# Optimization experiments

Measured on AMD Instinct MI355X. Metric: run time of the kernel, lower is better.

The kernel has to match this reference:

```python
import jax, jax.numpy as jnp
import numpy as np

NUM_HEADS = 32
NUM_KV_HEADS = 8
HEAD_DIM = 128
ROPE_THETA = 10000.0
HIDDEN = NUM_HEADS * HEAD_DIM


def setup_inputs() -> dict:
    key = jax.random.key(0)
    ks = jax.random.split(key, 5)
    B, S = 2, 2048
    hidden_states = jax.random.normal(ks[0], (B, S, HIDDEN), dtype=jnp.float32)
    wq = jax.random.normal(ks[1], (HIDDEN, HIDDEN), dtype=jnp.float32) * 0.02
    wk = jax.random.normal(ks[2], (NUM_KV_HEADS * HEAD_DIM, HIDDEN), dtype=jnp.float32) * 0.02
    wv = jax.random.normal(ks[3], (NUM_KV_HEADS * HEAD_DIM, HIDDEN), dtype=jnp.float32) * 0.02
    wo = jax.random.normal(ks[4], (HIDDEN, HIDDEN), dtype=jnp.float32) * 0.02
    position_ids = jnp.broadcast_to(jnp.arange(S, dtype=jnp.int64 if jax.config.read('jax_enable_x64') else jnp.int32)[None, :], (B, S))
    return {"hidden_states": hidden_states, "position_ids": position_ids,
            "wq": wq, "wk": wk, "wv": wv, "wo": wo}


def _rotate_half(x):
    x1, x2 = jnp.split(x, 2, axis=-1)
    return jnp.concatenate((-x2, x1), axis=-1)


def _rope_tables(position_ids, dtype):
    # inv_freq: [head_dim/2]
    inv_freq = 1.0 / (ROPE_THETA ** (jnp.arange(0, HEAD_DIM, 2, dtype=jnp.float32) / HEAD_DIM))
    # freqs per position: [B, S, head_dim/2] -> emb [B, S, head_dim]
    freqs = position_ids.astype(jnp.float32)[..., None] * inv_freq  # bsd2
    emb = jnp.concatenate((freqs, freqs), axis=-1)
    # unsqueeze head dim -> [B, 1, S, head_dim]
    return jnp.cos(emb).astype(dtype)[:, None], jnp.sin(emb).astype(dtype)[:, None]


def reference(hidden_states, position_ids, wq, wk, wv, wo):
    B, S, H = hidden_states.shape
    n_rep = NUM_HEADS // NUM_KV_HEADS
    # projections (torch Linear: x @ W^T)
    q = (hidden_states @ wq.T).reshape(B, S, NUM_HEADS, HEAD_DIM).transpose(0, 2, 1, 3)
    k = (hidden_states @ wk.T).reshape(B, S, NUM_KV_HEADS, HEAD_DIM).transpose(0, 2, 1, 3)
    v = (hidden_states @ wv.T).reshape(B, S, NUM_KV_HEADS, HEAD_DIM).transpose(0, 2, 1, 3)
    cos, sin = _rope_tables(position_ids, hidden_states.dtype)
    q = q * cos + _rotate_half(q) * sin
    k = k * cos + _rotate_half(k) * sin
    # repeat_kv: [B, kvH, S, D] -> [B, H, S, D]
    k = jnp.repeat(k, n_rep, axis=1)
    v = jnp.repeat(v, n_rep, axis=1)
    scale = 1.0 / jnp.sqrt(jnp.asarray(HEAD_DIM, dtype=hidden_states.dtype))
    scores = jnp.einsum('bhqd,bhkd->bhqk', q, k) * scale
    causal = jnp.tril(jnp.ones((S, S), dtype=bool))
    scores = jnp.where(causal[None, None], scores, jnp.finfo(scores.dtype).min)
    # softmax in fp32 then cast back (matches HF upcast)
    attn = jax.nn.softmax(scores.astype(jnp.float32), axis=-1).astype(q.dtype)
    out = jnp.einsum('bhqk,bhkd->bhqd', attn, v)
    out = out.transpose(0, 2, 1, 3).reshape(B, S, H)
    return out @ wo.T
```

## Files before the change

kernel.cpp:

```cpp
#include <hip/hip_runtime.h>
#include <stdint.h>

#define NH      32
#define NKVH    8
#define HD      128
#define BATCH   2
#define SEQ     2048
#define HIDDEN  4096
#define KVDIM   1024
#define TOKENS  (BATCH*SEQ)

typedef __bf16 bf16x8 __attribute__((ext_vector_type(8)));
typedef float  f32x4  __attribute__((ext_vector_type(4)));

__device__ __forceinline__ uint16_t f32_to_bf16(float f) {
  union { float f; uint32_t u; } v; v.f = f;
  uint32_t r = v.u + 0x7FFFu + ((v.u >> 16) & 1u);
  return (uint16_t)(r >> 16);
}
__device__ __forceinline__ float bf16_to_f32(uint16_t h) {
  union { uint32_t u; float f; } v; v.u = ((uint32_t)h) << 16;
  return v.f;
}
__device__ __forceinline__ bf16x8 ld_frag(const uint16_t* p) {
  return *(const bf16x8*)p;
}
#define MFMA_BF16(a,b,c) __builtin_amdgcn_mfma_f32_16x16x32_bf16((a),(b),(c),0,0,0)
#define NEG_BIG (-1.0e30f)

typedef __attribute__((address_space(1))) void as1_void;
typedef __attribute__((address_space(3))) void as3_void;
__device__ __forceinline__ void gload_lds16(const void* g, void* l) {
  __builtin_amdgcn_global_load_lds((as1_void*)g, (as3_void*)l, 16, 0, 0);
}

__device__ __forceinline__ void cvt8(const float* __restrict__ s,
                                     uint16_t* __restrict__ d, size_t i) {
  const float4* sp = (const float4*)s + 2*i;
  float4 a = sp[0], b = sp[1];
  union { uint16_t u[8]; uint4 v; } o;
  o.u[0]=f32_to_bf16(a.x); o.u[1]=f32_to_bf16(a.y);
  o.u[2]=f32_to_bf16(a.z); o.u[3]=f32_to_bf16(a.w);
  o.u[4]=f32_to_bf16(b.x); o.u[5]=f32_to_bf16(b.y);
  o.u[6]=f32_to_bf16(b.z); o.u[7]=f32_to_bf16(b.w);
  ((uint4*)d)[i] = o.v;
}

__global__ __launch_bounds__(256) void cvt_all(
    const float* __restrict__ X,  const float* __restrict__ Wq,
    const float* __restrict__ Wk, const float* __restrict__ Wv,
    uint16_t* __restrict__ R0, uint16_t* __restrict__ R1,
    uint16_t* __restrict__ R2, uint16_t* __restrict__ R3)
{
  int blk = blockIdx.x;
  const float* s; uint16_t* d; int b0;
  if (blk < 8192)       { s = X;  d = R0; b0 = 0; }
  else if (blk < 16384) { s = Wq; d = R1; b0 = 8192; }
  else if (blk < 18432) { s = Wk; d = R2; b0 = 16384; }
  else                  { s = Wv; d = R3; b0 = 18432; }
  cvt8(s, d, (size_t)(blk - b0)*256 + threadIdx.x);
}

__global__ __launch_bounds__(256) void cvt_one(
    const float* __restrict__ s, uint16_t* __restrict__ d)
{
  cvt8(s, d, (size_t)blockIdx.x*256 + threadIdx.x);
}

__device__ __forceinline__ void store_c(uint16_t* p, float v) { *p = f32_to_bf16(v); }
__device__ __forceinline__ void store_c(float*    p, float v) { *p = v; }

template <typename TC>
__device__ __forceinline__ void gemm_body(
    const uint16_t* __restrict__ A, const uint16_t* __restrict__ B,
    TC* __restrict__ C, int m0, int n0, int N, int K)
{
  __shared__ __align__(16) uint16_t As[3][128*32];
  __shared__ __align__(16) uint16_t Bs[3][128*32];
  const int tid  = threadIdx.x;
  const int wave = tid >> 6;
  const int lane = tid & 63;
  const int wm = (wave >> 1) * 64;
  const int wn = (wave & 1) * 64;
  const int srow = lane >> 2;
  const int scol = (((lane & 3) ^ ((lane >> 3) & 3)) * 8);
  const uint16_t* Ap = A + (size_t)(m0 + wave*16 + srow) * K + scol;
  const uint16_t* Bp = B + (size_t)(n0 + wave*16 + srow) * K + scol;
  const int wuo = wave*16*32;
  const int fr = lane & 15;
  const int fo = (((lane >> 4) ^ ((fr >> 1) & 3)) * 8);
  const int NT = K / 32;

  #pragma unroll
  for (int t = 0; t < 2; ++t) {
    gload_lds16(Ap + (size_t)t*32,                &As[t][wuo]);
    gload_lds16(Ap + (size_t)64*K + (size_t)t*32, &As[t][64*32 + wuo]);
    gload_lds16(Bp + (size_t)t*32,                &Bs[t][wuo]);
    gload_lds16(Bp + (size_t)64*K + (size_t)t*32, &Bs[t][64*32 + wuo]);
  }

  f32x4 acc[4][4] = {};
  int s_cur = 0, s_stage = 2;
  for (int t = 0; t < NT; ++t) {
    if (t < NT - 1) asm volatile("s_waitcnt vmcnt(4)" ::: "memory");
    else            asm volatile("s_waitcnt vmcnt(0)" ::: "memory");
    __builtin_amdgcn_s_barrier();
    asm volatile("" ::: "memory");

    if (t + 2 < NT) {
      const size_t k2 = (size_t)(t + 2) * 32;
      gload_lds16(Ap + k2,                &As[s_stage][wuo]);
      gload_lds16(Ap + (size_t)64*K + k2, &As[s_stage][64*32 + wuo]);
      gload_lds16(Bp + k2,                &Bs[s_stage][wuo]);
      gload_lds16(Bp + (size_t)64*K + k2, &Bs[s_stage][64*32 + wuo]);
    }

    const uint16_t* Asb = As[s_cur];
    const uint16_t* Bsb = Bs[s_cur];
    bf16x8 af[4], bfr[4];
    #pragma unroll
    for (int i = 0; i < 4; ++i) af[i]  = ld_frag(&Asb[(wm + i*16 + fr)*32 + fo]);
    #pragma unroll
    for (int j = 0; j < 4; ++j) bfr[j] = ld_frag(&Bsb[(wn + j*16 + fr)*32 + fo]);
    __builtin_amdgcn_s_setprio(1);
    #pragma unroll
    for (int i = 0; i < 4; ++i)
      #pragma unroll
      for (int j = 0; j < 4; ++j)
        acc[i][j] = MFMA_BF16(af[i], bfr[j], acc[i][j]);
    __builtin_amdgcn_s_setprio(0);

    s_cur   = (s_cur   == 2) ? 0 : s_cur + 1;
    s_stage = (s_stage == 2) ? 0 : s_stage + 1;
  }

  const int cr = (lane >> 4) * 4;
  const int cfr = lane & 15;
  #pragma unroll
  for (int i = 0; i < 4; ++i)
    #pragma unroll
    for (int j = 0; j < 4; ++j)
      #pragma unroll
      for (int r = 0; r < 4; ++r)
        store_c(&C[(size_t)(m0 + wm + i*16 + cr + r) * N + (n0 + wn + j*16 + cfr)],
                acc[i][j][r]);
}

__global__ __launch_bounds__(256, 3) void qkv_gemm(
    const uint16_t* __restrict__ X,
    const uint16_t* __restrict__ Wq, const uint16_t* __restrict__ Wk,
    const uint16_t* __restrict__ Wv,
    uint16_t* __restrict__ Qo, uint16_t* __restrict__ Ko, uint16_t* __restrict__ Vo)
{
  int bx = blockIdx.x;
  const uint16_t* B; uint16_t* C; int n0, N;
  if (bx < 32)      { B = Wq; C = Qo; n0 = bx*128;      N = HIDDEN; }
  else if (bx < 40) { B = Wk; C = Ko; n0 = (bx-32)*128; N = KVDIM;  }
  else              { B = Wv; C = Vo; n0 = (bx-40)*128; N = KVDIM;  }
  gemm_body<uint16_t>(X, B, C, blockIdx.y*128, n0, N, HIDDEN);
}

__global__ __launch_bounds__(256, 3) void out_gemm(
    const uint16_t* __restrict__ A, const uint16_t* __restrict__ B,
    float* __restrict__ C, int N, int K)
{
  gemm_body<float>(A, B, C, blockIdx.y*128, blockIdx.x*128, N, K);
}

__global__ __launch_bounds__(256) void rope_kernel(
    uint16_t* __restrict__ Q, uint16_t* __restrict__ K)
{
  int idx = blockIdx.x * 256 + threadIdx.x;
  int j = idx & 63;
  int rest = idx >> 6;
  int h = rest % (NH + NKVH);
  int t = rest / (NH + NKVH);
  float pos = (float)(t % SEQ);
  float inv_freq = __exp10f(-0.0625f * (float)j);
  float ang = pos * inv_freq;
  float s, c;
  __sincosf(ang, &s, &c);
  uint16_t* base = (h < NH) ? (Q + (size_t)t*HIDDEN + h*HD)
                            : (K + (size_t)t*KVDIM + (h-NH)*HD);
  float x1 = bf16_to_f32(base[j]);
  float x2 = bf16_to_f32(base[j+64]);
  base[j]    = f32_to_bf16(x1*c - x2*s);
  base[j+64] = f32_to_bf16(x2*c + x1*s);
}

__global__ __launch_bounds__(256) void transpose_v(
    const uint16_t* __restrict__ V, uint16_t* __restrict__ Vt)
{
  __shared__ uint16_t tile[64][66];
  int bh = blockIdx.z;  int b = bh >> 3, h = bh & 7;
  int s0 = blockIdx.x * 64;
  int d0 = blockIdx.y * 64;
  int tx = threadIdx.x & 63;
  int ty = threadIdx.x >> 6;
  const uint16_t* Vp = V + (size_t)b*SEQ*KVDIM + (size_t)h*HD;
  for (int r = ty; r < 64; r += 4)
    tile[r][tx] = Vp[(size_t)(s0 + r)*KVDIM + d0 + tx];
  __syncthreads();
  uint16_t* Vtp = Vt + ((size_t)b*NKVH + h)*HD*SEQ;
  for (int r = ty; r < 64; r += 4)
    Vtp[(size_t)(d0 + r)*SEQ + s0 + tx] = tile[tx][r];
}

#define KSTR 136
#define VSTR 72

__global__ __launch_bounds__(256, 4) void flash_attn(
    uint16_t* __restrict__ Q, const uint16_t* __restrict__ K,
    const uint16_t* __restrict__ Vt)
{
  __shared__ __align__(16) uint16_t Ks[64*KSTR];
  __shared__ __align__(16) uint16_t Vs[128*VSTR];
  uint16_t* Ps = Ks;

  const int tid  = threadIdx.x;
  const int wave = tid >> 6;
  const int lane = tid & 63;
  const int fr = lane & 15;
  const int g  = lane >> 4;
  const int fo = g * 8;
  const int bh = blockIdx.y;
  const int b = bh >> 5, h = bh & 31;
  const int kvh = h >> 2;

  uint16_t*       Qh = Q  + (size_t)b*SEQ*HIDDEN + (size_t)h*HD;
  const uint16_t* Kp = K  + (size_t)b*SEQ*KVDIM  + (size_t)kvh*HD;
  const uint16_t* Vp = Vt + ((size_t)b*NKVH + kvh)*HD*SEQ;

  #pragma unroll
  for (int pass = 0; pass < 2; ++pass) {
    const int qt = pass ? (31 - (int)blockIdx.x) : (int)blockIdx.x;
    const int q0 = qt * 64;
    const int qrow = q0 + wave*16 + fr;
    const int orow_base = q0 + wave*16 + g*4;

    bf16x8 qf[4];
    #pragma unroll
    for (int ks = 0; ks < 4; ++ks)
      qf[ks] = ld_frag(Qh + (size_t)(q0 + wave*16 + fr)*HIDDEN + ks*32 + fo);

    float m_i = NEG_BIG, l_i = 0.f;
    f32x4 oacc[8] = {};

    const int nkt = qt + 1;
    for (int kt = 0; kt < nkt; ++kt) {
      const int k0 = kt * 64;
      __syncthreads();
      #pragma unroll
      for (int i = 0; i < 4; ++i) {
        int gi = tid + i*256;
        int kr = gi >> 4, kc = (gi & 15) * 8;
        *(bf16x8*)&Ks[kr*KSTR + kc] = *(const bf16x8*)(Kp + (size_t)(k0 + kr)*KVDIM + kc);
        int vr = gi >> 3, vc = (gi & 7) * 8;
        *(bf16x8*)&Vs[vr*VSTR + vc] = *(const bf16x8*)(Vp + (size_t)vr*SEQ + k0 + vc);
      }
      __syncthreads();

      f32x4 sacc[4] = {};
      #pragma unroll
      for (int ks = 0; ks < 4; ++ks) {
        bf16x8 bk[4];
        #pragma unroll
        for (int j = 0; j < 4; ++j) bk[j] = ld_frag(&Ks[(j*16 + fr)*KSTR + ks*32 + fo]);
        __builtin_amdgcn_s_setprio(1);
        #pragma unroll
        for (int j = 0; j < 4; ++j) sacc[j] = MFMA_BF16(bk[j], qf[ks], sacc[j]);
        __builtin_amdgcn_s_setprio(0);
      }

      const bool diag = (kt == qt);
      #pragma unroll
      for (int j = 0; j < 4; ++j)
        #pragma unroll
        for (int r = 0; r < 4; ++r) {
          float v = sacc[j][r] * 0.08838834764831845f;
          if (diag && (k0 + j*16 + g*4 + r > qrow)) v = NEG_BIG;
          sacc[j][r] = v;
        }

      float mt = sacc[0][0];
      #pragma unroll
      for (int j = 0; j < 4; ++j)
        #pragma unroll
        for (int r = 0; r < 4; ++r)
          if (j | r) mt = fmaxf(mt, sacc[j][r]);
      mt = fmaxf(mt, __shfl_xor(mt, 16, 64));
      mt = fmaxf(mt, __shfl_xor(mt, 32, 64));

      float alpha = 1.0f;
      if (!__all(mt <= m_i + 8.0f)) {
        float mn = fmaxf(m_i, mt);
        alpha = __expf(m_i - mn);
        m_i = mn;
        #pragma unroll
        for (int r = 0; r < 4; ++r) {
          float ar = __shfl(alpha, g*4 + r, 64);
          #pragma unroll
          for (int n = 0; n < 8; ++n) oacc[n][r] *= ar;
        }
      }

      float lt = 0.f;
      uint2 pw[4];
      #pragma unroll
      for (int j = 0; j < 4; ++j) {
        float p0 = __expf(sacc[j][0] - m_i);
        float p1 = __expf(sacc[j][1] - m_i);
        float p2 = __expf(sacc[j][2] - m_i);
        float p3 = __expf(sacc[j][3] - m_i);
        lt += (p0 + p1) + (p2 + p3);
        union { uint16_t u[4]; uint2 v; } pk;
        pk.u[0] = f32_to_bf16(p0); pk.u[1] = f32_to_bf16(p1);
        pk.u[2] = f32_to_bf16(p2); pk.u[3] = f32_to_bf16(p3);
        pw[j] = pk.v;
      }
      lt += __shfl_xor(lt, 16, 64);
      lt += __shfl_xor(lt, 32, 64);
      l_i = l_i * alpha + lt;

      __syncthreads();

      #pragma unroll
      for (int j = 0; j < 4; ++j)
        *(uint2*)&Ps[(wave*16 + fr)*VSTR + j*16 + g*4] = pw[j];

      #pragma unroll
      for (int ks = 0; ks < 2; ++ks) {
        bf16x8 ap = ld_frag(&Ps[(wave*16 + fr)*VSTR + ks*32 + fo]);
        #pragma unroll
        for (int half = 0; half < 2; ++half) {
          bf16x8 bv[4];
          #pragma unroll
          for (int n = 0; n < 4; ++n)
            bv[n] = ld_frag(&Vs[((half*4 + n)*16 + fr)*VSTR + ks*32 + fo]);
          __builtin_amdgcn_s_setprio(1);
          #pragma unroll
          for (int n = 0; n < 4; ++n)
            oacc[half*4 + n] = MFMA_BF16(ap, bv[n], oacc[half*4 + n]);
          __builtin_amdgcn_s_setprio(0);
        }
      }
    }

    #pragma unroll
    for (int r = 0; r < 4; ++r) {
      float lr = __shfl(l_i, g*4 + r, 64);
      float inv_l = 1.0f / lr;
      #pragma unroll
      for (int n = 0; n < 8; ++n)
        Qh[(size_t)(orow_base + r)*HIDDEN + n*16 + fr] = f32_to_bf16(oacc[n][r] * inv_l);
    }
    __syncthreads();
  }
}

extern "C" void kernel_launch(void* const* d_in, const int* in_sizes, int n_in,
                              void* d_out, int out_size, void* d_ws, size_t ws_size,
                              hipStream_t stream)
{
  (void)in_sizes; (void)n_in; (void)out_size; (void)ws_size;
  const float* hidden = (const float*)d_in[0];
  const float* wq = (const float*)d_in[2];
  const float* wk = (const float*)d_in[3];
  const float* wv = (const float*)d_in[4];
  const float* wo = (const float*)d_in[5];
  float* out = (float*)d_out;

  uint16_t* R0 = (uint16_t*)d_ws;
  uint16_t* R1 = R0 + (size_t)HIDDEN*HIDDEN;
  uint16_t* R2 = R1 + (size_t)HIDDEN*HIDDEN;
  uint16_t* R3 = R2 + (size_t)KVDIM*HIDDEN;
  uint16_t* Qb = R3 + (size_t)KVDIM*HIDDEN;
  uint16_t* Kb = Qb + (size_t)TOKENS*HIDDEN;
  uint16_t* Vb = Kb + (size_t)TOKENS*KVDIM;

  dim3 blk(256);
  cvt_all<<<dim3(20480), blk, 0, stream>>>(hidden, wq, wk, wv, R0, R1, R2, R3);
  qkv_gemm<<<dim3(48, TOKENS/128), blk, 0, stream>>>(R0, R1, R2, R3, Qb, Kb, Vb);
  rope_kernel<<<dim3(TOKENS*(NH+NKVH)*64/256), blk, 0, stream>>>(Qb, Kb);
  cvt_one<<<dim3(HIDDEN*HIDDEN/8/256), blk, 0, stream>>>(wo, R0);
  transpose_v<<<dim3(SEQ/64, HD/64, BATCH*NKVH), blk, 0, stream>>>(Vb, R1);
  flash_attn<<<dim3(16, BATCH*NH), blk, 0, stream>>>(Qb, Kb, R1);
  out_gemm<<<dim3(HIDDEN/128, TOKENS/128), blk, 0, stream>>>(Qb, R0, out, HIDDEN, HIDDEN);
}
```

Measured before the change: 802.0 us.

## Use double-buffered GEMM body with higher occupancy for output projection

```diff
diff --git a/kernel.cpp b/kernel.cpp
--- a/kernel.cpp
+++ b/kernel.cpp
@@ -146,6 +146,75 @@
                 acc[i][j][r]);
 }
 
+template <typename TC>
+__device__ __forceinline__ void gemm_body2(
+    const uint16_t* __restrict__ A, const uint16_t* __restrict__ B,
+    TC* __restrict__ C, int m0, int n0, int N, int K)
+{
+  __shared__ __align__(16) uint16_t As[2][128*32];
+  __shared__ __align__(16) uint16_t Bs[2][128*32];
+  const int tid  = threadIdx.x;
+  const int wave = tid >> 6;
+  const int lane = tid & 63;
+  const int wm = (wave >> 1) * 64;
+  const int wn = (wave & 1) * 64;
+  const int srow = lane >> 2;
+  const int scol = (((lane & 3) ^ ((lane >> 3) & 3)) * 8);
+  const uint16_t* Ap = A + (size_t)(m0 + wave*16 + srow) * K + scol;
+  const uint16_t* Bp = B + (size_t)(n0 + wave*16 + srow) * K + scol;
+  const int wuo = wave*16*32;
+  const int fr = lane & 15;
+  const int fo = (((lane >> 4) ^ ((fr >> 1) & 3)) * 8);
+  const int NT = K / 32;
+
+  gload_lds16(Ap,                &As[0][wuo]);
+  gload_lds16(Ap + (size_t)64*K, &As[0][64*32 + wuo]);
+  gload_lds16(Bp,                &Bs[0][wuo]);
+  gload_lds16(Bp + (size_t)64*K, &Bs[0][64*32 + wuo]);
+
+  f32x4 acc[4][4] = {};
+  for (int t = 0; t < NT; ++t) {
+    asm volatile("s_waitcnt vmcnt(0)" ::: "memory");
+    __builtin_amdgcn_s_barrier();
+    asm volatile("" ::: "memory");
+
+    if (t + 1 < NT) {
+      const int s = (t + 1) & 1;
+      const size_t k1 = (size_t)(t + 1) * 32;
+      gload_lds16(Ap + k1,                &As[s][wuo]);
+      gload_lds16(Ap + (size_t)64*K + k1, &As[s][64*32 + wuo]);
+      gload_lds16(Bp + k1,                &Bs[s][wuo]);
+      gload_lds16(Bp + (size_t)64*K + k1, &Bs[s][64*32 + wuo]);
+    }
+
+    const uint16_t* Asb = As[t & 1];
+    const uint16_t* Bsb = Bs[t & 1];
+    bf16x8 af[4], bfr[4];
+    #pragma unroll
+    for (int i = 0; i < 4; ++i) af[i]  = ld_frag(&Asb[(wm + i*16 + fr)*32 + fo]);
+    #pragma unroll
+    for (int j = 0; j < 4; ++j) bfr[j] = ld_frag(&Bsb[(wn + j*16 + fr)*32 + fo]);
+    __builtin_amdgcn_s_setprio(1);
+    #pragma unroll
+    for (int i = 0; i < 4; ++i)
+      #pragma unroll
+      for (int j = 0; j < 4; ++j)
+        acc[i][j] = MFMA_BF16(af[i], bfr[j], acc[i][j]);
+    __builtin_amdgcn_s_setprio(0);
+  }
+
+  const int cr = (lane >> 4) * 4;
+  const int cfr = lane & 15;
+  #pragma unroll
+  for (int i = 0; i < 4; ++i)
+    #pragma unroll
+    for (int j = 0; j < 4; ++j)
+      #pragma unroll
+      for (int r = 0; r < 4; ++r)
+        store_c(&C[(size_t)(m0 + wm + i*16 + cr + r) * N + (n0 + wn + j*16 + cfr)],
+                acc[i][j][r]);
+}
+
 __global__ __launch_bounds__(256, 3) void qkv_gemm(
     const uint16_t* __restrict__ X,
     const uint16_t* __restrict__ Wq, const uint16_t* __restrict__ Wk,
@@ -160,11 +229,11 @@
   gemm_body<uint16_t>(X, B, C, blockIdx.y*128, n0, N, HIDDEN);
 }
 
-__global__ __launch_bounds__(256, 3) void out_gemm(
+__global__ __launch_bounds__(256, 4) void out_gemm(
     const uint16_t* __restrict__ A, const uint16_t* __restrict__ B,
     float* __restrict__ C, int N, int K)
 {
-  gemm_body<float>(A, B, C, blockIdx.y*128, blockIdx.x*128, N, K);
+  gemm_body2<float>(A, B, C, blockIdx.y*128, blockIdx.x*128, N, K);
 }
 
 __global__ __launch_bounds__(256) void rope_kernel(
```

Measured after the change: 770.5 us. 1.04x faster.
